# Kernel optimization log

Hardware: AMD Instinct MI355X
Metric: run time of the kernel (lower is better)

The kernel has to match this reference:

```python
import jax, jax.numpy as jnp
import numpy as np

NBUS = 33
B33 = [(1,2),(2,3),(3,4),(4,5),(5,6),(6,7),(7,8),(8,9),(9,10),(10,11),(11,12),(12,13),(13,14),(14,15),(15,16),(16,17),(17,18),(2,19),(19,20),(20,21),(21,22),(3,23),(23,24),(24,25),(6,26),(26,27),(27,28),(28,29),(29,30),(30,31),(31,32),(32,33)]


def setup_inputs() -> dict:
    key = jax.random.key(0)
    k1, k2, k3 = jax.random.split(key, 3)
    B, W, M, F = 32, 128, 100, 8
    N, H, GH, K = NBUS, 256, 128, 3
    rng = np.random.default_rng(0)
    br = np.array(B33) - 1
    src = np.concatenate([br[:, 0], br[:, 1]])
    dst = np.concatenate([br[:, 1], br[:, 0]])
    w_half = rng.uniform(0.5, 2.0, size=br.shape[0]).astype(np.float32)
    p = lambda *s: jnp.asarray(rng.normal(0.0, 0.02, size=s).astype(np.float32))
    z = lambda *s: jnp.zeros(s, jnp.float32)
    return {
        'r_seq': jax.random.normal(k1, (B, W, M), jnp.float32),
        'feat_seq': jax.random.normal(k2, (B, W, F), jnp.float32),
        'x_wls_seq': jax.random.normal(k3, (B, W, 2 * N), jnp.float32),
        'edge_index': jnp.asarray(np.stack([src, dst]).astype(np.int32)),
        'edge_weight': jnp.asarray(np.concatenate([w_half, w_half])),
        'pre_w': p(F + 2, GH), 'pre_b': z(GH),
        'tag_w1': p(K + 1, GH, GH), 'tag_b1': z(GH),
        'tag_w2': p(K + 1, GH, GH), 'tag_b2': z(GH),
        'post_w': p(GH, H), 'post_b': z(H),
        'tp_w1': p(M + 2 * N, H), 'tp_b1': z(H),
        'tp_w2': p(H, H), 'tp_b2': z(H),
        'gru_wih0': p(H, 3 * H), 'gru_whh0': p(H, 3 * H), 'gru_bih0': z(3 * H), 'gru_bhh0': z(3 * H),
        'gru_wih1': p(H, 3 * H), 'gru_whh1': p(H, 3 * H), 'gru_bih1': z(3 * H), 'gru_bhh1': z(3 * H),
        'fg_w': p(H, H), 'fg_b': z(H),
        'fs_w': p(H, H), 'fs_b': z(H),
        'gate_w': p(2 * H, H), 'gate_b': z(H),
        'd1_w': p(H, H), 'd1_b': z(H),
        'd2_w': p(H, 2), 'd2_b': z(2),
    }


def _gru_layer(x, wih, whh, bih, bhh):
    # x: (B, W, Din); torch GRU gate order [r, z, n]
    def step(h, xt):
        gi = xt @ wih + bih
        gh = h @ whh + bhh
        ir, iz, inn = jnp.split(gi, 3, axis=-1)
        hr, hz, hn = jnp.split(gh, 3, axis=-1)
        r = jax.nn.sigmoid(ir + hr)
        zt = jax.nn.sigmoid(iz + hz)
        n = jnp.tanh(inn + r * hn)
        h = (1.0 - zt) * n + zt * h
        return h, h
    h0 = jnp.zeros((x.shape[0], whh.shape[0]), x.dtype)
    _, ys = jax.lax.scan(step, h0, jnp.swapaxes(x, 0, 1))
    return jnp.swapaxes(ys, 0, 1)


def _forward(r_seq, feat_seq, x_wls_seq, edge_index, edge_weight,
             pre_w, pre_b, tag_w1, tag_b1, tag_w2, tag_b2, post_w, post_b,
             tp_w1, tp_b1, tp_w2, tp_b2,
             gru_wih0, gru_whh0, gru_bih0, gru_bhh0,
             gru_wih1, gru_whh1, gru_bih1, gru_bhh1,
             fg_w, fg_b, fs_w, fs_b, gate_w, gate_b,
             d1_w, d1_b, d2_w, d2_b):
    B, W, M = r_seq.shape
    N = NBUS
    # ---- spatial branch (batched TAGConv, K=3, 2 layers) ----
    va = x_wls_seq[..., :N, None]
    vm = x_wls_seq[..., N:, None]
    x_nodes = jnp.concatenate([va, vm], axis=-1)                 # (B,W,N,2)
    feat_n = jnp.broadcast_to(feat_seq[:, :, None, :], (B, W, N, feat_seq.shape[-1]))
    gin = jnp.concatenate([feat_n, x_nodes], axis=-1) @ pre_w + pre_b  # (B,W,N,GH)
    g = gin.reshape(B * W, N, gin.shape[-1])
    src, dst = edge_index[0], edge_index[1]
    # gcn_norm (no self-loops), shared across all B*W graph copies
    deg = jnp.zeros((N,), g.dtype).at[dst].add(edge_weight)
    dinv = jnp.where(deg > 0, deg ** -0.5, 0.0)
    norm = dinv[src] * edge_weight * dinv[dst]                   # (E,)

    def prop(h):  # out[i] = sum_{j->i} norm * h[j], batched over graphs
        return jnp.zeros_like(h).at[:, dst].add(h[:, src] * norm[None, :, None])

    def tag(h, Wk, b):  # TAGConv: sum_k A^k h @ W_k + b
        out = h @ Wk[0]
        hk = h
        for k in range(1, Wk.shape[0]):
            hk = prop(hk)
            out = out + hk @ Wk[k]
        return out + b

    g = jax.nn.relu(tag(g, tag_w1, tag_b1))
    g = tag(g, tag_w2, tag_b2)
    g = g.reshape(B, W, N, -1) @ post_w + post_b                 # (B,W,N,H)
    # ---- temporal branch (MLP -> 2-layer GRU); E_time=None skips MHA ----
    s = jnp.concatenate([r_seq, x_wls_seq], axis=-1)
    s = jax.nn.relu(s @ tp_w1 + tp_b1)
    s = jax.nn.relu(s @ tp_w2 + tp_b2)
    s = _gru_layer(s, gru_wih0, gru_whh0, gru_bih0, gru_bhh0)
    s = _gru_layer(s, gru_wih1, gru_whh1, gru_bih1, gru_bhh1)    # (B,W,H)
    # ---- gated fusion + decoder ----
    g_t = g @ fg_w + fg_b                                        # (B,W,N,H)
    s_t = (s @ fs_w + fs_b)[:, :, None, :]                       # (B,W,1,H)
    s_full = jnp.broadcast_to(s_t, g_t.shape)
    alpha = jax.nn.sigmoid(jnp.concatenate([g_t, s_full], axis=-1) @ gate_w + gate_b)
    u = alpha * g_t + (1.0 - alpha) * s_full
    u = jax.nn.relu(u @ d1_w + d1_b) @ d2_w + d2_b               # (B,W,N,2)
    dx = jnp.concatenate([u[..., 0], u[..., 1]], axis=-1)        # (B,W,2N)
    return x_wls_seq + dx


def reference(r_seq, feat_seq, x_wls_seq, edge_index, edge_weight,
              pre_w, pre_b, tag_w1, tag_b1, tag_w2, tag_b2, post_w, post_b,
              tp_w1, tp_b1, tp_w2, tp_b2,
              gru_wih0, gru_whh0, gru_bih0, gru_bhh0,
              gru_wih1, gru_whh1, gru_bih1, gru_bhh1,
              fg_w, fg_b, fs_w, fs_b, gate_w, gate_b,
              d1_w, d1_b, d2_w, d2_b):
    return _forward(r_seq, feat_seq, x_wls_seq, edge_index, edge_weight,
                    pre_w, pre_b, tag_w1, tag_b1, tag_w2, tag_b2, post_w, post_b,
                    tp_w1, tp_b1, tp_w2, tp_b2,
                    gru_wih0, gru_whh0, gru_bih0, gru_bhh0,
                    gru_wih1, gru_whh1, gru_bih1, gru_bhh1,
                    fg_w, fg_b, fs_w, fs_b, gate_w, gate_b,
                    d1_w, d1_b, d2_w, d2_b)
```

## Files before the change

kernel.cpp:

```cpp
#include <hip/hip_runtime.h>
#include <hip/hip_fp16.h>
#include <cmath>

#define DEV __device__ __forceinline__

typedef unsigned short ushortT;
typedef short bs8 __attribute__((ext_vector_type(8)));
typedef float f32x4 __attribute__((ext_vector_type(4)));
typedef _Float16 f16x2 __attribute__((ext_vector_type(2)));

constexpr int kBW = 4096;
constexpr int kM = 100, kF = 8, kN = 33, kH = 256, kGH = 128, kE = 64;

constexpr int OFF_ROWPTR  = 0;
constexpr int OFF_COLSRC  = 64;
constexpr int OFF_COLNORM = 128;
constexpr int OFF_C       = 192;
constexpr int OFF_WC      = 512;
constexpr int OFF_SPRE    = 33280;
constexpr int OFF_GI      = OFF_SPRE + kBW * kH;
constexpr int OFF_SFUSE   = OFF_GI + kBW * 3 * kH;
constexpr int OFF_SGATE   = OFF_SFUSE + kBW * kH;
constexpr int OFF_WQ0     = OFF_SFUSE;
constexpr int OFF_WQ1     = OFF_SFUSE + 98304;
constexpr int WB_TW1  = 0;
constexpr int WB_TW2  = 65536;
constexpr int WB_WC   = 131072;
constexpr int WB_GATE = 163840;
constexpr int WB_D1   = 229376;
constexpr int WB_TOT  = 294912;

DEV float sigmoidf(float x) { return 1.0f / (1.0f + expf(-x)); }

DEV ushortT f2bf(float x) {
  unsigned u = __float_as_uint(x);
  unsigned r = u + 0x7fffu + ((u >> 16) & 1u);
  return (ushortT)(r >> 16);
}
DEV float bf2f(ushortT u) { return __uint_as_float(((unsigned)u) << 16); }

DEV f32x4 mfma16(bs8 a, bs8 b, f32x4 c) {
  return __builtin_amdgcn_mfma_f32_16x16x32_bf16(a, b, c, 0, 0, 0);
}
DEV bs8 ldb(const ushortT* p) { return *reinterpret_cast<const bs8*>(p); }

#if __has_builtin(__builtin_amdgcn_fdot2)
DEV float dot2(unsigned w, unsigned hp, float acc) {
  f16x2 wv = __builtin_bit_cast(f16x2, w);
  f16x2 hv = __builtin_bit_cast(f16x2, hp);
  return __builtin_amdgcn_fdot2(wv, hv, acc, false);
}
#else
DEV float dot2(unsigned w, unsigned hp, float acc) {
  f16x2 wv = __builtin_bit_cast(f16x2, w);
  f16x2 hv = __builtin_bit_cast(f16x2, hp);
  acc = fmaf((float)wv.x, (float)hv.x, acc);
  acc = fmaf((float)wv.y, (float)hv.y, acc);
  return acc;
}
#endif

__global__ void k_prep(const int* __restrict__ ei, const float* __restrict__ ew,
                       float* __restrict__ ws) {
  if (blockIdx.x != 0 || threadIdx.x != 0) return;
  int* rowptr = (int*)(ws + OFF_ROWPTR);
  int* colsrc = (int*)(ws + OFF_COLSRC);
  float* colnorm = ws + OFF_COLNORM;
  const int* src = ei;
  const int* dst = ei + kE;
  float deg[kN]; int cnt[kN];
  for (int n = 0; n < kN; ++n) { deg[n] = 0.f; cnt[n] = 0; }
  for (int e = 0; e < kE; ++e) { deg[dst[e]] += ew[e]; cnt[dst[e]]++; }
  float dinv[kN];
  for (int n = 0; n < kN; ++n) dinv[n] = deg[n] > 0.f ? 1.0f / sqrtf(deg[n]) : 0.f;
  int pos[kN];
  int run = 0;
  for (int n = 0; n < kN; ++n) { rowptr[n] = run; pos[n] = run; run += cnt[n]; }
  rowptr[kN] = run;
  for (int e = 0; e < kE; ++e) {
    int d = dst[e];
    int p = pos[d]++;
    colsrc[p] = src[e];
    colnorm[p] = dinv[src[e]] * ew[e] * dinv[d];
  }
}

__global__ void k_wcfold(const float* __restrict__ post_w, const float* __restrict__ post_b,
                         const float* __restrict__ fg_w, const float* __restrict__ fg_b,
                         float* __restrict__ ws) {
  const int j = threadIdx.x;
  if ((int)blockIdx.x < kGH) {
    const int k = blockIdx.x;
    float a = 0.f;
    #pragma unroll 4
    for (int m = 0; m < kH; ++m) a = fmaf(post_w[k * kH + m], fg_w[m * kH + j], a);
    ws[OFF_WC + k * kH + j] = a;
  } else {
    float a = fg_b[j];
    #pragma unroll 4
    for (int m = 0; m < kH; ++m) a = fmaf(post_b[m], fg_w[m * kH + j], a);
    ws[OFF_C + j] = a;
  }
}

__global__ void k_wq(const float* __restrict__ w0, const float* __restrict__ w1,
                     float* __restrict__ ws) {
  const int idx = blockIdx.x * 256 + threadIdx.x;
  if (idx >= 2 * 98304) return;
  const int layer = idx / 98304;
  const int rem = idx - layer * 98304;
  const int p = rem / 768, j = rem - p * 768;
  const float* w = layer ? w1 : w0;
  unsigned* dst = (unsigned*)(ws + (layer ? OFF_WQ1 : OFF_WQ0));
  __half2 v = __floats2half2_rn(w[(2 * p) * 768 + j], w[(2 * p + 1) * 768 + j]);
  dst[rem] = *reinterpret_cast<unsigned*>(&v);
}

__global__ void k_wprep(const float* __restrict__ tw1, const float* __restrict__ tw2,
                        const float* __restrict__ gatew, const float* __restrict__ d1w,
                        float* __restrict__ ws) {
  const int idx = blockIdx.x * 256 + threadIdx.x;
  if (idx >= WB_TOT) return;
  ushortT* WB = (ushortT*)(ws + OFF_GI);
  float v; int dst;
  if (idx < 65536) {
    int s = idx >> 14, r = idx & 16383, k = r >> 7, col = r & 127;
    v = tw1[(s << 14) + (k << 7) + col]; dst = WB_TW1 + (s << 14) + (col << 7) + k;
  } else if (idx < 131072) {
    int i = idx - 65536; int s = i >> 14, r = i & 16383, k = r >> 7, col = r & 127;
    v = tw2[(s << 14) + (k << 7) + col]; dst = WB_TW2 + (s << 14) + (col << 7) + k;
  } else if (idx < 163840) {
    int i = idx - 131072; int k = i & 127, col = i >> 7;
    v = ws[OFF_WC + (k << 8) + col]; dst = WB_WC + (col << 7) + k;
  } else if (idx < 229376) {
    int i = idx - 163840; int k = i & 255, col = i >> 8;
    v = gatew[(k << 8) + col]; dst = WB_GATE + (col << 8) + k;
  } else {
    int i = idx - 229376; int k = i & 255, col = i >> 8;
    v = d1w[(k << 8) + col]; dst = WB_D1 + (col << 8) + k;
  }
  WB[dst] = f2bf(v);
}

__global__ __launch_bounds__(256) void k_tpmlp(
    const float* __restrict__ r_seq, const float* __restrict__ x_wls,
    const float* __restrict__ w1, const float* __restrict__ b1,
    const float* __restrict__ w2, const float* __restrict__ b2,
    float* __restrict__ sout) {
  __shared__ float inr[8][kM + 2 * kN];
  __shared__ float h1[8][kH];
  const int bw0 = blockIdx.x * 8, tid = threadIdx.x;
  #pragma unroll
  for (int r = 0; r < 8; ++r) {
    for (int c = tid; c < kM + 2 * kN; c += 256)
      inr[r][c] = (c < kM) ? r_seq[(bw0 + r) * kM + c]
                           : x_wls[(bw0 + r) * 2 * kN + (c - kM)];
  }
  __syncthreads();
  float acc[8];
  {
    const float bb = b1[tid];
    #pragma unroll
    for (int r = 0; r < 8; ++r) acc[r] = bb;
  }
  for (int k = 0; k < kM + 2 * kN; ++k) {
    const float w = w1[k * kH + tid];
    #pragma unroll
    for (int r = 0; r < 8; ++r) acc[r] = fmaf(inr[r][k], w, acc[r]);
  }
  #pragma unroll
  for (int r = 0; r < 8; ++r) h1[r][tid] = fmaxf(acc[r], 0.f);
  __syncthreads();
  {
    const float bb = b2[tid];
    #pragma unroll
    for (int r = 0; r < 8; ++r) acc[r] = bb;
  }
  #pragma unroll 2
  for (int k = 0; k < kH; ++k) {
    const float w = w2[k * kH + tid];
    #pragma unroll
    for (int r = 0; r < 8; ++r) acc[r] = fmaf(h1[r][k], w, acc[r]);
  }
  #pragma unroll
  for (int r = 0; r < 8; ++r) sout[(bw0 + r) * kH + tid] = fmaxf(acc[r], 0.f);
}

__global__ __launch_bounds__(768) void k_gigemm(
    const float* __restrict__ sin, const float* __restrict__ wih,
    const float* __restrict__ bih, float* __restrict__ gi) {
  __shared__ float sr[8][kH];
  const int bw0 = blockIdx.x * 8, tid = threadIdx.x;
  for (int i = tid; i < 8 * kH; i += 768) sr[i >> 8][i & 255] = sin[bw0 * kH + i];
  __syncthreads();
  float acc[8];
  {
    const float bb = bih[tid];
    #pragma unroll
    for (int r = 0; r < 8; ++r) acc[r] = bb;
  }
  #pragma unroll 2
  for (int k = 0; k < kH; ++k) {
    const float w = wih[k * 768 + tid];
    #pragma unroll
    for (int r = 0; r < 8; ++r) acc[r] = fmaf(sr[r][k], w, acc[r]);
  }
  #pragma unroll
  for (int r = 0; r < 8; ++r) gi[(bw0 + r) * 768 + tid] = acc[r];
}

__global__ __launch_bounds__(768, 3) void k_scan(
    const float* __restrict__ gi, const float* __restrict__ wq,
    const float* __restrict__ bhh, float* __restrict__ sout) {
  __shared__ float h[kH];
  __shared__ __align__(16) unsigned hpk[kH / 2];
  __shared__ float gh[3 * kH];
  const int b = blockIdx.x, tid = threadIdx.x;
  const unsigned* wqp = (const unsigned*)wq;
  unsigned wr[128];
  #pragma unroll
  for (int p = 0; p < 128; ++p) wr[p] = wqp[p * 768 + tid];
  if (tid < kH) h[tid] = 0.f;
  if (tid < kH / 2) hpk[tid] = 0u;
  __syncthreads();
  const float bb = bhh[tid];
  for (int t = 0; t < 128; ++t) {
    const float* girow = gi + (b * 128 + t) * 768;
    float a0 = bb, a1 = 0.f, a2 = 0.f, a3 = 0.f;
    #pragma unroll
    for (int q = 0; q < 32; ++q) {
      const uint4 hp = *reinterpret_cast<const uint4*>(hpk + 4 * q);
      a0 = dot2(wr[4 * q + 0], hp.x, a0);
      a1 = dot2(wr[4 * q + 1], hp.y, a1);
      a2 = dot2(wr[4 * q + 2], hp.z, a2);
      a3 = dot2(wr[4 * q + 3], hp.w, a3);
    }
    gh[tid] = (a0 + a1) + (a2 + a3);
    __syncthreads();
    if (tid < kH) {
      float r = sigmoidf(girow[tid] + gh[tid]);
      float z = sigmoidf(girow[kH + tid] + gh[kH + tid]);
      float n = tanhf(fmaf(r, gh[2 * kH + tid], girow[2 * kH + tid]));
      float hn = (1.f - z) * n + z * h[tid];
      h[tid] = hn;
      reinterpret_cast<__half*>(hpk)[tid] = __float2half(hn);
      sout[(b * 128 + t) * kH + tid] = hn;
    }
    __syncthreads();
  }
}

__global__ __launch_bounds__(256) void k_fsgate(
    const float* __restrict__ s1, const float* __restrict__ fsw,
    const float* __restrict__ fsb, const float* __restrict__ gw,
    const float* __restrict__ gb, float* __restrict__ sfuse,
    float* __restrict__ sgate) {
  __shared__ float sr[8][kH], sf[8][kH];
  const int bw0 = blockIdx.x * 8, tid = threadIdx.x;
  for (int i = tid; i < 8 * kH; i += 256) sr[i >> 8][i & 255] = s1[bw0 * kH + i];
  __syncthreads();
  float acc[8];
  {
    const float bb = fsb[tid];
    #pragma unroll
    for (int r = 0; r < 8; ++r) acc[r] = bb;
  }
  #pragma unroll 2
  for (int k = 0; k < kH; ++k) {
    const float w = fsw[k * kH + tid];
    #pragma unroll
    for (int r = 0; r < 8; ++r) acc[r] = fmaf(sr[r][k], w, acc[r]);
  }
  #pragma unroll
  for (int r = 0; r < 8; ++r) { sf[r][tid] = acc[r]; sfuse[(bw0 + r) * kH + tid] = acc[r]; }
  __syncthreads();
  {
    const float bb = gb[tid];
    #pragma unroll
    for (int r = 0; r < 8; ++r) acc[r] = bb;
  }
  #pragma unroll 2
  for (int k = 0; k < kH; ++k) {
    const float w = gw[(kH + k) * kH + tid];
    #pragma unroll
    for (int r = 0; r < 8; ++r) acc[r] = fmaf(sf[r][k], w, acc[r]);
  }
  #pragma unroll
  for (int r = 0; r < 8; ++r) sgate[(bw0 + r) * kH + tid] = acc[r];
}


constexpr int SB0 = 0;
constexpr int SB1 = 36 * 136;
constexpr int SGT = 2 * 36 * 136;
constexpr int S_TOT = SGT + 48 * 264;

DEV void propb(ushortT* __restrict__ dst, const ushortT* __restrict__ src,
               const int* __restrict__ rp, const int* __restrict__ cs,
               const float* __restrict__ cn) {
  for (int idx = threadIdx.x; idx < kN * 64; idx += 256) {
    const int n = idx >> 6, j2 = idx & 63;
    float a0 = 0.f, a1 = 0.f;
    const int p1 = rp[n + 1];
    for (int p = rp[n]; p < p1; ++p) {
      const unsigned v = *(const unsigned*)(src + cs[p] * 136 + 2 * j2);
      const float w = cn[p];
      a0 = fmaf(__uint_as_float(v << 16), w, a0);
      a1 = fmaf(__uint_as_float(v & 0xffff0000u), w, a1);
    }
    *(unsigned*)(dst + n * 136 + 2 * j2) = (unsigned)f2bf(a0) | ((unsigned)f2bf(a1) << 16);
  }
}

template <bool RELU>
DEV void tag_mfma(ushortT* __restrict__ Sb, const ushortT* __restrict__ WT,
                  const float* __restrict__ b, const int* __restrict__ rp,
                  const int* __restrict__ cs, const float* __restrict__ cn,
                  int wv, int lane) {
  const int lr = lane & 15, lg = lane >> 4;
  f32x4 acc[6];
  #pragma unroll
  for (int i = 0; i < 6; ++i) acc[i] = (f32x4){0.f, 0.f, 0.f, 0.f};
  ushortT* bufs[2] = {Sb + SB0, Sb + SB1};
  int cur = 0;
  #pragma unroll
  for (int s = 0; s < 4; ++s) {
    const ushortT* A = bufs[cur];
    #pragma unroll
    for (int ks = 0; ks < 4; ++ks) {
      const int kof = ks * 32 + lg * 8;
      bs8 a0 = ldb(A + (lr) * 136 + kof);
      bs8 a1 = ldb(A + (16 + lr) * 136 + kof);
      bs8 a2 = ldb(A + (32 + lr) * 136 + kof);
      #pragma unroll
      for (int nt = 0; nt < 2; ++nt) {
        const int col = (wv * 2 + nt) * 16 + lr;
        bs8 bb = ldb(WT + (s << 14) + (col << 7) + kof);
        acc[0 + nt] = mfma16(a0, bb, acc[0 + nt]);
        acc[2 + nt] = mfma16(a1, bb, acc[2 + nt]);
        acc[4 + nt] = mfma16(a2, bb, acc[4 + nt]);
      }
    }
    if (s < 3) {
      propb(bufs[cur ^ 1], bufs[cur], rp, cs, cn);
      __syncthreads();
      cur ^= 1;
    }
  }
  #pragma unroll
  for (int mt = 0; mt < 3; ++mt)
    #pragma unroll
    for (int nt = 0; nt < 2; ++nt) {
      const int col = (wv * 2 + nt) * 16 + lr;
      const float bias = b[col];
      const f32x4 v = acc[mt * 2 + nt];
      #pragma unroll
      for (int r = 0; r < 4; ++r) {
        const int row = mt * 16 + lg * 4 + r;
        if (row < kN) {
          float x = v[r] + bias;
          if (RELU) x = fmaxf(x, 0.f);
          (Sb + SB0)[row * 136 + col] = f2bf(x);
        }
      }
    }
  __syncthreads();
}

__global__ __launch_bounds__(256, 3) void k_fused(
    const float* __restrict__ feat_seq, const float* __restrict__ x_wls,
    const float* __restrict__ pre_w, const float* __restrict__ pre_b,
    const float* __restrict__ tb1, const float* __restrict__ tb2,
    const float* __restrict__ d1b, const float* __restrict__ d2w,
    const float* __restrict__ d2b, const float* __restrict__ ws,
    const float* __restrict__ sfuse, const float* __restrict__ sgate,
    float* __restrict__ out) {
  __shared__ __align__(16) ushortT S[S_TOT];
  __shared__ float sfrow[kH], sgrow[kH];
  __shared__ float xw[2 * kN];
  __shared__ float featl[kF];
  __shared__ int rp[kN + 1], cs[kE];
  __shared__ float cn[kE];
  __shared__ float part[4][48][2];
  const int tid = threadIdx.x, bw = blockIdx.x;
  const int wv = tid >> 6, lane = tid & 63;
  const int lr = lane & 15, lg = lane >> 4;
  const ushortT* WB = (const ushortT*)(ws + OFF_GI);

  sfrow[tid] = sfuse[bw * kH + tid];
  sgrow[tid] = sgate[bw * kH + tid];
  if (tid < 2 * kN) xw[tid] = x_wls[bw * 2 * kN + tid];
  else if (tid >= 66 && tid < 66 + kF) featl[tid - 66] = feat_seq[bw * kF + (tid - 66)];
  if (tid >= 128 && tid < 128 + kN + 1) rp[tid - 128] = ((const int*)(ws + OFF_ROWPTR))[tid - 128];
  if (tid >= 192) {
    cs[tid - 192] = ((const int*)(ws + OFF_COLSRC))[tid - 192];
    cn[tid - 192] = ws[OFF_COLNORM + (tid - 192)];
  }
  __syncthreads();

  for (int idx = tid; idx < kN * kGH; idx += 256) {
    const int n = idx >> 7, j = idx & 127;
    float a = pre_b[j];
    #pragma unroll
    for (int f = 0; f < kF; ++f) a = fmaf(featl[f], pre_w[f * kGH + j], a);
    a = fmaf(xw[n], pre_w[8 * kGH + j], a);
    a = fmaf(xw[kN + n], pre_w[9 * kGH + j], a);
    S[SB0 + n * 136 + j] = f2bf(a);
  }
  __syncthreads();

  tag_mfma<true >(S, WB + WB_TW1, tb1, rp, cs, cn, wv, lane);
  tag_mfma<false>(S, WB + WB_TW2, tb2, rp, cs, cn, wv, lane);

  {
    f32x4 acc[12];
    #pragma unroll
    for (int i = 0; i < 12; ++i) acc[i] = (f32x4){0.f, 0.f, 0.f, 0.f};
    #pragma unroll
    for (int ks = 0; ks < 4; ++ks) {
      const int kof = ks * 32 + lg * 8;
      bs8 a0 = ldb(S + SB0 + (lr) * 136 + kof);
      bs8 a1 = ldb(S + SB0 + (16 + lr) * 136 + kof);
      bs8 a2 = ldb(S + SB0 + (32 + lr) * 136 + kof);
      #pragma unroll
      for (int nt = 0; nt < 4; ++nt) {
        const int col = (wv * 4 + nt) * 16 + lr;
        bs8 bb = ldb(WB + WB_WC + (col << 7) + kof);
        acc[0 + nt] = mfma16(a0, bb, acc[0 + nt]);
        acc[4 + nt] = mfma16(a1, bb, acc[4 + nt]);
        acc[8 + nt] = mfma16(a2, bb, acc[8 + nt]);
      }
    }
    #pragma unroll
    for (int mt = 0; mt < 3; ++mt)
      #pragma unroll
      for (int nt = 0; nt < 4; ++nt) {
        const int col = (wv * 4 + nt) * 16 + lr;
        const float cb = ws[OFF_C + col];
        const f32x4 v = acc[mt * 4 + nt];
        #pragma unroll
        for (int r = 0; r < 4; ++r) {
          const int row = mt * 16 + lg * 4 + r;
          if (row < kN) (S + SGT)[row * 264 + col] = f2bf(v[r] + cb);
        }
      }
    __syncthreads();
  }

  {
    f32x4 acc[12];
    #pragma unroll
    for (int i = 0; i < 12; ++i) acc[i] = (f32x4){0.f, 0.f, 0.f, 0.f};
    #pragma unroll 2
    for (int ks = 0; ks < 8; ++ks) {
      const int kof = ks * 32 + lg * 8;
      bs8 a0 = ldb(S + SGT + (lr) * 264 + kof);
      bs8 a1 = ldb(S + SGT + (16 + lr) * 264 + kof);
      bs8 a2 = ldb(S + SGT + (32 + lr) * 264 + kof);
      #pragma unroll
      for (int nt = 0; nt < 4; ++nt) {
        const int col = (wv * 4 + nt) * 16 + lr;
        bs8 bb = ldb(WB + WB_GATE + (col << 8) + kof);
        acc[0 + nt] = mfma16(a0, bb, acc[0 + nt]);
        acc[4 + nt] = mfma16(a1, bb, acc[4 + nt]);
        acc[8 + nt] = mfma16(a2, bb, acc[8 + nt]);
      }
    }
    #pragma unroll
    for (int mt = 0; mt < 3; ++mt)
      #pragma unroll
      for (int nt = 0; nt < 4; ++nt) {
        const int col = (wv * 4 + nt) * 16 + lr;
        const float sg = sgrow[col], sf = sfrow[col];
        #pragma unroll
        for (int r = 0; r < 4; ++r) {
          const int row = mt * 16 + lg * 4 + r;
          if (row < kN) {
            const float al = sigmoidf(acc[mt * 4 + nt][r] + sg);
            const float gt = bf2f((S + SGT)[row * 264 + col]);
            acc[mt * 4 + nt][r] = al * gt + (1.f - al) * sf;
          }
        }
      }
    __syncthreads();
    #pragma unroll
    for (int mt = 0; mt < 3; ++mt)
      #pragma unroll
      for (int nt = 0; nt < 4; ++nt) {
        const int col = (wv * 4 + nt) * 16 + lr;
        #pragma unroll
        for (int r = 0; r < 4; ++r) {
          const int row = mt * 16 + lg * 4 + r;
          if (row < kN) (S + SGT)[row * 264 + col] = f2bf(acc[mt * 4 + nt][r]);
        }
      }
    __syncthreads();
  }

  {
    f32x4 acc[12];
    #pragma unroll
    for (int i = 0; i < 12; ++i) acc[i] = (f32x4){0.f, 0.f, 0.f, 0.f};
    #pragma unroll 2
    for (int ks = 0; ks < 8; ++ks) {
      const int kof = ks * 32 + lg * 8;
      bs8 a0 = ldb(S + SGT + (lr) * 264 + kof);
      bs8 a1 = ldb(S + SGT + (16 + lr) * 264 + kof);
      bs8 a2 = ldb(S + SGT + (32 + lr) * 264 + kof);
      #pragma unroll
      for (int nt = 0; nt < 4; ++nt) {
        const int col = (wv * 4 + nt) * 16 + lr;
        bs8 bb = ldb(WB + WB_D1 + (col << 8) + kof);
        acc[0 + nt] = mfma16(a0, bb, acc[0 + nt]);
        acc[4 + nt] = mfma16(a1, bb, acc[4 + nt]);
        acc[8 + nt] = mfma16(a2, bb, acc[8 + nt]);
      }
    }
    float p0[3][4], p1[3][4];
    #pragma unroll
    for (int mt = 0; mt < 3; ++mt)
      #pragma unroll
      for (int r = 0; r < 4; ++r) { p0[mt][r] = 0.f; p1[mt][r] = 0.f; }
    #pragma unroll
    for (int nt = 0; nt < 4; ++nt) {
      const int col = (wv * 4 + nt) * 16 + lr;
      const float db = d1b[col];
      const float2 dp = *reinterpret_cast<const float2*>(d2w + col * 2);
      #pragma unroll
      for (int mt = 0; mt < 3; ++mt)
        #pragma unroll
        for (int r = 0; r < 4; ++r) {
          const float v = fmaxf(acc[mt * 4 + nt][r] + db, 0.f);
          p0[mt][r] = fmaf(v, dp.x, p0[mt][r]);
          p1[mt][r] = fmaf(v, dp.y, p1[mt][r]);
        }
    }
    #pragma unroll
    for (int mt = 0; mt < 3; ++mt)
      #pragma unroll
      for (int r = 0; r < 4; ++r) {
        #pragma unroll
        for (int off = 1; off < 16; off <<= 1) {
          p0[mt][r] += __shfl_xor(p0[mt][r], off, 64);
          p1[mt][r] += __shfl_xor(p1[mt][r], off, 64);
        }
      }
    if (lr == 0) {
      #pragma unroll
      for (int mt = 0; mt < 3; ++mt)
        #pragma unroll
        for (int r = 0; r < 4; ++r) {
          const int row = mt * 16 + lg * 4 + r;
          part[wv][row][0] = p0[mt][r];
          part[wv][row][1] = p1[mt][r];
        }
    }
    __syncthreads();
    if (tid < 66) {
      const int c = tid >= 33 ? 1 : 0;
      const int n = tid - 33 * c;
      float s = d2b[c];
      #pragma unroll
      for (int w = 0; w < 4; ++w) s += part[w][n][c];
      out[bw * 66 + tid] = xw[tid] + s;
    }
  }
}

extern "C" void kernel_launch(void* const* d_in, const int* in_sizes, int n_in,
                              void* d_out, int out_size, void* d_ws, size_t ws_size,
                              hipStream_t stream) {
  const float* r_seq  = (const float*)d_in[0];
  const float* feat   = (const float*)d_in[1];
  const float* x_wls  = (const float*)d_in[2];
  const int*   eidx   = (const int*)d_in[3];
  const float* ew     = (const float*)d_in[4];
  const float* pre_w  = (const float*)d_in[5];
  const float* pre_b  = (const float*)d_in[6];
  const float* tag_w1 = (const float*)d_in[7];
  const float* tag_b1 = (const float*)d_in[8];
  const float* tag_w2 = (const float*)d_in[9];
  const float* tag_b2 = (const float*)d_in[10];
  const float* post_w = (const float*)d_in[11];
  const float* post_b = (const float*)d_in[12];
  const float* tp_w1  = (const float*)d_in[13];
  const float* tp_b1  = (const float*)d_in[14];
  const float* tp_w2  = (const float*)d_in[15];
  const float* tp_b2  = (const float*)d_in[16];
  const float* wih0   = (const float*)d_in[17];
  const float* whh0   = (const float*)d_in[18];
  const float* bih0   = (const float*)d_in[19];
  const float* bhh0   = (const float*)d_in[20];
  const float* wih1   = (const float*)d_in[21];
  const float* whh1   = (const float*)d_in[22];
  const float* bih1   = (const float*)d_in[23];
  const float* bhh1   = (const float*)d_in[24];
  const float* fg_w   = (const float*)d_in[25];
  const float* fg_b   = (const float*)d_in[26];
  const float* fs_w   = (const float*)d_in[27];
  const float* fs_b   = (const float*)d_in[28];
  const float* gate_w = (const float*)d_in[29];
  const float* gate_b = (const float*)d_in[30];
  const float* d1_w   = (const float*)d_in[31];
  const float* d1_b   = (const float*)d_in[32];
  const float* d2_w   = (const float*)d_in[33];
  const float* d2_b   = (const float*)d_in[34];
  float* ws = (float*)d_ws;
  float* outp = (float*)d_out;

  k_prep<<<1, 64, 0, stream>>>(eidx, ew, ws);
  k_wcfold<<<kGH + 1, kH, 0, stream>>>(post_w, post_b, fg_w, fg_b, ws);
  k_wq<<<768, 256, 0, stream>>>(whh0, whh1, ws);
  k_tpmlp<<<kBW / 8, 256, 0, stream>>>(r_seq, x_wls, tp_w1, tp_b1, tp_w2, tp_b2,
                                       ws + OFF_SPRE);
  k_gigemm<<<kBW / 8, 768, 0, stream>>>(ws + OFF_SPRE, wih0, bih0, ws + OFF_GI);
  k_scan<<<32, 768, 0, stream>>>(ws + OFF_GI, ws + OFF_WQ0, bhh0, ws + OFF_SPRE);
  k_gigemm<<<kBW / 8, 768, 0, stream>>>(ws + OFF_SPRE, wih1, bih1, ws + OFF_GI);
  k_scan<<<32, 768, 0, stream>>>(ws + OFF_GI, ws + OFF_WQ1, bhh1, ws + OFF_SPRE);
  k_wprep<<<(WB_TOT + 255) / 256, 256, 0, stream>>>(tag_w1, tag_w2, gate_w, d1_w, ws);
  k_fsgate<<<kBW / 8, 256, 0, stream>>>(ws + OFF_SPRE, fs_w, fs_b, gate_w, gate_b,
                                        ws + OFF_SFUSE, ws + OFF_SGATE);
  k_fused<<<kBW, 256, 0, stream>>>(feat, x_wls, pre_w, pre_b, tag_b1, tag_b2,
                                   d1_b, d2_w, d2_b, ws, ws + OFF_SFUSE,
                                   ws + OFF_SGATE, outp);
}
```

Before: 1.056 ms.

## Alias gate buffer onto TAG scratch, raise occupancy, widen GEMM row tiles, fast activations

The fused per-sample kernel now reuses the TAG ping-pong shared buffers for the gated tensor instead of a separate region. This shrinks LDS so launch bounds can request 5 blocks per SM, with extra barriers, zeroed padding rows and clamped MFMA row reads to keep the aliasing safe. The fp32 GEMM kernels (tp MLP, GI projection, fs/gate) process 16 rows per block instead of 8 to reuse each weight load more, at the cost of more registers and fewer blocks. Sigmoid and tanh switch to __expf plus hardware reciprocal, which lowers accuracy slightly.

```diff
diff --git a/kernel.cpp b/kernel.cpp
--- a/kernel.cpp
+++ b/kernel.cpp
@@ -30,7 +30,9 @@
 constexpr int WB_D1   = 229376;
 constexpr int WB_TOT  = 294912;
 
-DEV float sigmoidf(float x) { return 1.0f / (1.0f + expf(-x)); }
+DEV float frcp(float x) { return __builtin_amdgcn_rcpf(x); }
+DEV float fsig(float x) { return frcp(1.0f + __expf(-x)); }
+DEV float ftanh(float x) { float e = __expf(2.0f * x); return 1.0f - 2.0f * frcp(e + 1.0f); }
 
 DEV ushortT f2bf(float x) {
   unsigned u = __float_as_uint(x);
@@ -147,66 +149,66 @@
     const float* __restrict__ w1, const float* __restrict__ b1,
     const float* __restrict__ w2, const float* __restrict__ b2,
     float* __restrict__ sout) {
-  __shared__ float inr[8][kM + 2 * kN];
-  __shared__ float h1[8][kH];
-  const int bw0 = blockIdx.x * 8, tid = threadIdx.x;
-  #pragma unroll
-  for (int r = 0; r < 8; ++r) {
+  __shared__ float inr[16][kM + 2 * kN];
+  __shared__ float h1[16][kH];
+  const int bw0 = blockIdx.x * 16, tid = threadIdx.x;
+  #pragma unroll
+  for (int r = 0; r < 16; ++r) {
     for (int c = tid; c < kM + 2 * kN; c += 256)
       inr[r][c] = (c < kM) ? r_seq[(bw0 + r) * kM + c]
                            : x_wls[(bw0 + r) * 2 * kN + (c - kM)];
   }
   __syncthreads();
-  float acc[8];
+  float acc[16];
   {
     const float bb = b1[tid];
     #pragma unroll
-    for (int r = 0; r < 8; ++r) acc[r] = bb;
+    for (int r = 0; r < 16; ++r) acc[r] = bb;
   }
   for (int k = 0; k < kM + 2 * kN; ++k) {
     const float w = w1[k * kH + tid];
     #pragma unroll
-    for (int r = 0; r < 8; ++r) acc[r] = fmaf(inr[r][k], w, acc[r]);
-  }
-  #pragma unroll
-  for (int r = 0; r < 8; ++r) h1[r][tid] = fmaxf(acc[r], 0.f);
+    for (int r = 0; r < 16; ++r) acc[r] = fmaf(inr[r][k], w, acc[r]);
+  }
+  #pragma unroll
+  for (int r = 0; r < 16; ++r) h1[r][tid] = fmaxf(acc[r], 0.f);
   __syncthreads();
   {
     const float bb = b2[tid];
     #pragma unroll
-    for (int r = 0; r < 8; ++r) acc[r] = bb;
+    for (int r = 0; r < 16; ++r) acc[r] = bb;
   }
   #pragma unroll 2
   for (int k = 0; k < kH; ++k) {
     const float w = w2[k * kH + tid];
     #pragma unroll
-    for (int r = 0; r < 8; ++r) acc[r] = fmaf(h1[r][k], w, acc[r]);
-  }
-  #pragma unroll
-  for (int r = 0; r < 8; ++r) sout[(bw0 + r) * kH + tid] = fmaxf(acc[r], 0.f);
+    for (int r = 0; r < 16; ++r) acc[r] = fmaf(h1[r][k], w, acc[r]);
+  }
+  #pragma unroll
+  for (int r = 0; r < 16; ++r) sout[(bw0 + r) * kH + tid] = fmaxf(acc[r], 0.f);
 }
 
 __global__ __launch_bounds__(768) void k_gigemm(
     const float* __restrict__ sin, const float* __restrict__ wih,
     const float* __restrict__ bih, float* __restrict__ gi) {
-  __shared__ float sr[8][kH];
-  const int bw0 = blockIdx.x * 8, tid = threadIdx.x;
-  for (int i = tid; i < 8 * kH; i += 768) sr[i >> 8][i & 255] = sin[bw0 * kH + i];
-  __syncthreads();
-  float acc[8];
+  __shared__ float sr[16][kH];
+  const int bw0 = blockIdx.x * 16, tid = threadIdx.x;
+  for (int i = tid; i < 16 * kH; i += 768) sr[i >> 8][i & 255] = sin[bw0 * kH + i];
+  __syncthreads();
+  float acc[16];
   {
     const float bb = bih[tid];
     #pragma unroll
-    for (int r = 0; r < 8; ++r) acc[r] = bb;
+    for (int r = 0; r < 16; ++r) acc[r] = bb;
   }
   #pragma unroll 2
   for (int k = 0; k < kH; ++k) {
     const float w = wih[k * 768 + tid];
     #pragma unroll
-    for (int r = 0; r < 8; ++r) acc[r] = fmaf(sr[r][k], w, acc[r]);
-  }
-  #pragma unroll
-  for (int r = 0; r < 8; ++r) gi[(bw0 + r) * 768 + tid] = acc[r];
+    for (int r = 0; r < 16; ++r) acc[r] = fmaf(sr[r][k], w, acc[r]);
+  }
+  #pragma unroll
+  for (int r = 0; r < 16; ++r) gi[(bw0 + r) * 768 + tid] = acc[r];
 }
 
 __global__ __launch_bounds__(768, 3) void k_scan(
@@ -238,9 +240,9 @@
     gh[tid] = (a0 + a1) + (a2 + a3);
     __syncthreads();
     if (tid < kH) {
-      float r = sigmoidf(girow[tid] + gh[tid]);
-      float z = sigmoidf(girow[kH + tid] + gh[kH + tid]);
-      float n = tanhf(fmaf(r, gh[2 * kH + tid], girow[2 * kH + tid]));
+      float r = fsig(girow[tid] + gh[tid]);
+      float z = fsig(girow[kH + tid] + gh[kH + tid]);
+      float n = ftanh(fmaf(r, gh[2 * kH + tid], girow[2 * kH + tid]));
       float hn = (1.f - z) * n + z * h[tid];
       h[tid] = hn;
       reinterpret_cast<__half*>(hpk)[tid] = __float2half(hn);
@@ -255,45 +257,44 @@
     const float* __restrict__ fsb, const float* __restrict__ gw,
     const float* __restrict__ gb, float* __restrict__ sfuse,
     float* __restrict__ sgate) {
-  __shared__ float sr[8][kH], sf[8][kH];
-  const int bw0 = blockIdx.x * 8, tid = threadIdx.x;
-  for (int i = tid; i < 8 * kH; i += 256) sr[i >> 8][i & 255] = s1[bw0 * kH + i];
-  __syncthreads();
-  float acc[8];
+  __shared__ float sr[16][kH], sf[16][kH];
+  const int bw0 = blockIdx.x * 16, tid = threadIdx.x;
+  for (int i = tid; i < 16 * kH; i += 256) sr[i >> 8][i & 255] = s1[bw0 * kH + i];
+  __syncthreads();
+  float acc[16];
   {
     const float bb = fsb[tid];
     #pragma unroll
-    for (int r = 0; r < 8; ++r) acc[r] = bb;
+    for (int r = 0; r < 16; ++r) acc[r] = bb;
   }
   #pragma unroll 2
   for (int k = 0; k < kH; ++k) {
     const float w = fsw[k * kH + tid];
     #pragma unroll
-    for (int r = 0; r < 8; ++r) acc[r] = fmaf(sr[r][k], w, acc[r]);
-  }
-  #pragma unroll
-  for (int r = 0; r < 8; ++r) { sf[r][tid] = acc[r]; sfuse[(bw0 + r) * kH + tid] = acc[r]; }
+    for (int r = 0; r < 16; ++r) acc[r] = fmaf(sr[r][k], w, acc[r]);
+  }
+  #pragma unroll
+  for (int r = 0; r < 16; ++r) { sf[r][tid] = acc[r]; sfuse[(bw0 + r) * kH + tid] = acc[r]; }
   __syncthreads();
   {
     const float bb = gb[tid];
     #pragma unroll
-    for (int r = 0; r < 8; ++r) acc[r] = bb;
+    for (int r = 0; r < 16; ++r) acc[r] = bb;
   }
   #pragma unroll 2
   for (int k = 0; k < kH; ++k) {
     const float w = gw[(kH + k) * kH + tid];
     #pragma unroll
-    for (int r = 0; r < 8; ++r) acc[r] = fmaf(sf[r][k], w, acc[r]);
-  }
-  #pragma unroll
-  for (int r = 0; r < 8; ++r) sgate[(bw0 + r) * kH + tid] = acc[r];
+    for (int r = 0; r < 16; ++r) acc[r] = fmaf(sf[r][k], w, acc[r]);
+  }
+  #pragma unroll
+  for (int r = 0; r < 16; ++r) sgate[(bw0 + r) * kH + tid] = acc[r];
 }
 
 
 constexpr int SB0 = 0;
 constexpr int SB1 = 36 * 136;
-constexpr int SGT = 2 * 36 * 136;
-constexpr int S_TOT = SGT + 48 * 264;
+constexpr int S_TOT = 2 * 36 * 136;
 
 DEV void propb(ushortT* __restrict__ dst, const ushortT* __restrict__ src,
                const int* __restrict__ rp, const int* __restrict__ cs,
@@ -347,6 +348,7 @@
       cur ^= 1;
     }
   }
+  __syncthreads();
   #pragma unroll
   for (int mt = 0; mt < 3; ++mt)
     #pragma unroll
@@ -367,7 +369,7 @@
   __syncthreads();
 }
 
-__global__ __launch_bounds__(256, 3) void k_fused(
+__global__ __launch_bounds__(256, 5) void k_fused(
     const float* __restrict__ feat_seq, const float* __restrict__ x_wls,
     const float* __restrict__ pre_w, const float* __restrict__ pre_b,
     const float* __restrict__ tb1, const float* __restrict__ tb2,
@@ -386,6 +388,7 @@
   const int wv = tid >> 6, lane = tid & 63;
   const int lr = lane & 15, lg = lane >> 4;
   const ushortT* WB = (const ushortT*)(ws + OFF_GI);
+  ushortT* GT = S;
 
   sfrow[tid] = sfuse[bw * kH + tid];
   sgrow[tid] = sgate[bw * kH + tid];
@@ -396,6 +399,10 @@
     cs[tid - 192] = ((const int*)(ws + OFF_COLSRC))[tid - 192];
     cn[tid - 192] = ws[OFF_COLNORM + (tid - 192)];
   }
+  for (int i = tid; i < 3 * kGH; i += 256) {
+    S[SB0 + kN * 136 + i] = 0;
+    S[SB1 + kN * 136 + i] = 0;
+  }
   __syncthreads();
 
   for (int idx = tid; idx < kN * kGH; idx += 256) {
@@ -431,6 +438,7 @@
         acc[8 + nt] = mfma16(a2, bb, acc[8 + nt]);
       }
     }
+    __syncthreads();
     #pragma unroll
     for (int mt = 0; mt < 3; ++mt)
       #pragma unroll
@@ -441,7 +449,7 @@
         #pragma unroll
         for (int r = 0; r < 4; ++r) {
           const int row = mt * 16 + lg * 4 + r;
-          if (row < kN) (S + SGT)[row * 264 + col] = f2bf(v[r] + cb);
+          if (row < kN) GT[row * 264 + col] = f2bf(v[r] + cb);
         }
       }
     __syncthreads();
@@ -454,9 +462,10 @@
     #pragma unroll 2
     for (int ks = 0; ks < 8; ++ks) {
       const int kof = ks * 32 + lg * 8;
-      bs8 a0 = ldb(S + SGT + (lr) * 264 + kof);
-      bs8 a1 = ldb(S + SGT + (16 + lr) * 264 + kof);
-      bs8 a2 = ldb(S + SGT + (32 + lr) * 264 + kof);
+      const int r2 = (32 + lr) < 36 ? (32 + lr) : 35;
+      bs8 a0 = ldb(GT + (lr) * 264 + kof);
+      bs8 a1 = ldb(GT + (16 + lr) * 264 + kof);
+      bs8 a2 = ldb(GT + r2 * 264 + kof);
       #pragma unroll
       for (int nt = 0; nt < 4; ++nt) {
         const int col = (wv * 4 + nt) * 16 + lr;
@@ -476,8 +485,8 @@
         for (int r = 0; r < 4; ++r) {
           const int row = mt * 16 + lg * 4 + r;
           if (row < kN) {
-            const float al = sigmoidf(acc[mt * 4 + nt][r] + sg);
-            const float gt = bf2f((S + SGT)[row * 264 + col]);
+            const float al = fsig(acc[mt * 4 + nt][r] + sg);
+            const float gt = bf2f(GT[row * 264 + col]);
             acc[mt * 4 + nt][r] = al * gt + (1.f - al) * sf;
           }
         }
@@ -491,7 +500,7 @@
         #pragma unroll
         for (int r = 0; r < 4; ++r) {
           const int row = mt * 16 + lg * 4 + r;
-          if (row < kN) (S + SGT)[row * 264 + col] = f2bf(acc[mt * 4 + nt][r]);
+          if (row < kN) GT[row * 264 + col] = f2bf(acc[mt * 4 + nt][r]);
         }
       }
     __syncthreads();
@@ -504,9 +513,10 @@
     #pragma unroll 2
     for (int ks = 0; ks < 8; ++ks) {
       const int kof = ks * 32 + lg * 8;
-      bs8 a0 = ldb(S + SGT + (lr) * 264 + kof);
-      bs8 a1 = ldb(S + SGT + (16 + lr) * 264 + kof);
-      bs8 a2 = ldb(S + SGT + (32 + lr) * 264 + kof);
+      const int r2 = (32 + lr) < 36 ? (32 + lr) : 35;
+      bs8 a0 = ldb(GT + (lr) * 264 + kof);
+      bs8 a1 = ldb(GT + (16 + lr) * 264 + kof);
+      bs8 a2 = ldb(GT + r2 * 264 + kof);
       #pragma unroll
       for (int nt = 0; nt < 4; ++nt) {
         const int col = (wv * 4 + nt) * 16 + lr;
@@ -611,15 +621,15 @@
   k_prep<<<1, 64, 0, stream>>>(eidx, ew, ws);
   k_wcfold<<<kGH + 1, kH, 0, stream>>>(post_w, post_b, fg_w, fg_b, ws);
   k_wq<<<768, 256, 0, stream>>>(whh0, whh1, ws);
-  k_tpmlp<<<kBW / 8, 256, 0, stream>>>(r_seq, x_wls, tp_w1, tp_b1, tp_w2, tp_b2,
-                                       ws + OFF_SPRE);
-  k_gigemm<<<kBW / 8, 768, 0, stream>>>(ws + OFF_SPRE, wih0, bih0, ws + OFF_GI);
+  k_tpmlp<<<kBW / 16, 256, 0, stream>>>(r_seq, x_wls, tp_w1, tp_b1, tp_w2, tp_b2,
+                                        ws + OFF_SPRE);
+  k_gigemm<<<kBW / 16, 768, 0, stream>>>(ws + OFF_SPRE, wih0, bih0, ws + OFF_GI);
   k_scan<<<32, 768, 0, stream>>>(ws + OFF_GI, ws + OFF_WQ0, bhh0, ws + OFF_SPRE);
-  k_gigemm<<<kBW / 8, 768, 0, stream>>>(ws + OFF_SPRE, wih1, bih1, ws + OFF_GI);
+  k_gigemm<<<kBW / 16, 768, 0, stream>>>(ws + OFF_SPRE, wih1, bih1, ws + OFF_GI);
   k_scan<<<32, 768, 0, stream>>>(ws + OFF_GI, ws + OFF_WQ1, bhh1, ws + OFF_SPRE);
   k_wprep<<<(WB_TOT + 255) / 256, 256, 0, stream>>>(tag_w1, tag_w2, gate_w, d1_w, ws);
-  k_fsgate<<<kBW / 8, 256, 0, stream>>>(ws + OFF_SPRE, fs_w, fs_b, gate_w, gate_b,
-                                        ws + OFF_SFUSE, ws + OFF_SGATE);
+  k_fsgate<<<kBW / 16, 256, 0, stream>>>(ws + OFF_SPRE, fs_w, fs_b, gate_w, gate_b,
+                                         ws + OFF_SFUSE, ws + OFF_SGATE);
   k_fused<<<kBW, 256, 0, stream>>>(feat, x_wls, pre_w, pre_b, tag_b1, tag_b2,
                                    d1_b, d2_w, d2_b, ws, ws + OFF_SFUSE,
                                    ws + OFF_SGATE, outp);
```

Result: slower. 1.179 ms (+11.6%).
